# Optimization experiments

Measured on AMD Instinct MI355X. Metric: run time of the kernel, lower is better.

## Reference

```python
import jax, jax.numpy as jnp
import numpy as np

IN_F, OUT_F, N_TOK = 4096, 4096, 8192

def setup_inputs() -> dict:
    key = jax.random.key(0)
    k1, k2, k3 = jax.random.split(key, 3)
    x = jax.random.normal(k1, (N_TOK, IN_F), dtype=jnp.float32)
    scaler = jax.random.uniform(k2, (1,), dtype=jnp.float32)
    int8_weights = jax.random.randint(k3, (IN_F, OUT_F), -128, 128, dtype=jnp.int32)
    return {"x": x, "scaler": scaler, "int8_weights": int8_weights}

def reference(x, scaler, int8_weights):
    # dequantize int8 weights: fp_w = int8_w * scaler, then GEMM
    fp_weights = int8_weights.astype(x.dtype) * scaler  # [in, out]
    return jnp.matmul(x, fp_weights)  # [tokens, out]
```

## Files before the change

kernel.cpp:

```cpp
#include <hip/hip_runtime.h>

#define M_DIM 8192
#define N_DIM 4096
#define K_DIM 4096

typedef __attribute__((ext_vector_type(8))) __bf16 bf16x8;
typedef __attribute__((ext_vector_type(4))) float f32x4;
typedef __attribute__((ext_vector_type(8))) unsigned short u16x8;

typedef const __attribute__((address_space(1))) unsigned int gu32_t;
typedef __attribute__((address_space(3))) unsigned int lu32_t;

static __device__ __forceinline__ unsigned short f2bf(float f) {
    union { float f; unsigned int u; } v; v.f = f;
    unsigned int u = v.u;
    return (unsigned short)((u + 0x7fffu + ((u >> 16) & 1u)) >> 16);
}

#define X_BLOCKS 32768

__global__ __launch_bounds__(256) void prep_kernel(const float* __restrict__ x,
                                                   unsigned short* __restrict__ xb,
                                                   const int* __restrict__ w,
                                                   unsigned short* __restrict__ wt) {
    __shared__ unsigned short t[64][72];
    const int tid = threadIdx.x;
    if (blockIdx.x < X_BLOCKS) {
        size_t g = (size_t)blockIdx.x * 256 + tid;
        float4 a = ((const float4*)x)[g];
        ushort4 o;
        o.x = f2bf(a.x); o.y = f2bf(a.y); o.z = f2bf(a.z); o.w = f2bf(a.w);
        ((ushort4*)xb)[g] = o;
    } else {
        int bid = blockIdx.x - X_BLOCKS;
        int n0 = (bid & 63) * 64;
        int k0 = (bid >> 6) * 64;
#pragma unroll
        for (int i = 0; i < 16; i++) {
            int idx = tid + i * 256;
            int r = idx >> 6, c = idx & 63;
            int v = w[(size_t)(k0 + r) * N_DIM + n0 + c];
            t[c][r] = f2bf((float)v);
        }
        __syncthreads();
#pragma unroll
        for (int i = 0; i < 2; i++) {
            int slot = tid + i * 256;
            int r = slot >> 3, c = (slot & 7) * 8;
            u16x8 o = *(const u16x8*)&t[r][c];
            *(u16x8*)&wt[(size_t)(n0 + r) * K_DIM + k0 + c] = o;
        }
    }
}

static __device__ __forceinline__ int swz(int m) { return (m + (m >> 2)) & 3; }

__global__ __launch_bounds__(256) void gemm_bt_kernel(const unsigned short* __restrict__ A,
                                                      const unsigned short* __restrict__ B,
                                                      const float* __restrict__ scaler,
                                                      float* __restrict__ C) {
    __shared__ unsigned short As[128 * 32];
    __shared__ unsigned short Bs[128 * 32];

    const int tid  = threadIdx.x;
    const int m0   = blockIdx.y * 128;
    const int n0   = blockIdx.x * 128;
    const int wave = tid >> 6, lane = tid & 63;
    const int quad = lane >> 4, lr = lane & 15;
    const int wm   = wave >> 1, wn = wave & 1;

    const int q0 = tid, q1 = tid + 256;
    const int r0 = q0 >> 2, kc0 = (q0 & 3) ^ swz(r0);
    const int r1 = q1 >> 2, kc1 = (q1 & 3) ^ swz(r1);
    const unsigned short* ga0 = A + (size_t)(m0 + r0) * K_DIM + kc0 * 8;
    const unsigned short* ga1 = A + (size_t)(m0 + r1) * K_DIM + kc1 * 8;
    const unsigned short* gb0 = B + (size_t)(n0 + r0) * K_DIM + kc0 * 8;
    const unsigned short* gb1 = B + (size_t)(n0 + r1) * K_DIM + kc1 * 8;
    unsigned short* la0 = As + q0 * 8;
    unsigned short* la1 = As + q1 * 8;
    unsigned short* lb0 = Bs + q0 * 8;
    unsigned short* lb1 = Bs + q1 * 8;

    f32x4 acc[4][4];
#pragma unroll
    for (int i = 0; i < 4; i++)
#pragma unroll
        for (int j = 0; j < 4; j++) acc[i][j] = (f32x4){0.f, 0.f, 0.f, 0.f};

    const int swa = quad ^ swz(wm * 64 + lr);
    const int swb = quad ^ swz(wn * 64 + lr);
    const unsigned short* pa = &As[((wm * 64 + lr) * 4 + swa) * 8];
    const unsigned short* pb = &Bs[((wn * 64 + lr) * 4 + swb) * 8];

    for (int kt = 0; kt < K_DIM / 32; ++kt) {
        __builtin_amdgcn_global_load_lds((gu32_t*)ga0, (lu32_t*)la0, 16, 0, 0);
        __builtin_amdgcn_global_load_lds((gu32_t*)ga1, (lu32_t*)la1, 16, 0, 0);
        __builtin_amdgcn_global_load_lds((gu32_t*)gb0, (lu32_t*)lb0, 16, 0, 0);
        __builtin_amdgcn_global_load_lds((gu32_t*)gb1, (lu32_t*)lb1, 16, 0, 0);
        ga0 += 32; ga1 += 32; gb0 += 32; gb1 += 32;
        __syncthreads();

        bf16x8 af[4], bf[4];
#pragma unroll
        for (int mi = 0; mi < 4; mi++) af[mi] = *(const bf16x8*)(pa + mi * 512);
#pragma unroll
        for (int ni = 0; ni < 4; ni++) bf[ni] = *(const bf16x8*)(pb + ni * 512);

#pragma unroll
        for (int mi = 0; mi < 4; mi++)
#pragma unroll
            for (int ni = 0; ni < 4; ni++)
                acc[mi][ni] = __builtin_amdgcn_mfma_f32_16x16x32_bf16(
                    af[mi], bf[ni], acc[mi][ni], 0, 0, 0);
        __syncthreads();
    }

    const float s = scaler[0];
#pragma unroll
    for (int mi = 0; mi < 4; mi++)
#pragma unroll
        for (int ni = 0; ni < 4; ni++) {
            const int row = m0 + wm * 64 + mi * 16 + quad * 4;
            const int col = n0 + wn * 64 + ni * 16 + lr;
            float* cp = C + (size_t)row * N_DIM + col;
#pragma unroll
            for (int r = 0; r < 4; r++)
                cp[(size_t)r * N_DIM] = acc[mi][ni][r] * s;
        }
}

extern "C" void kernel_launch(void* const* d_in, const int* in_sizes, int n_in,
                              void* d_out, int out_size, void* d_ws, size_t ws_size,
                              hipStream_t stream) {
    const float* x      = (const float*)d_in[0];
    const float* scaler = (const float*)d_in[1];
    const int*   w      = (const int*)d_in[2];
    float*       out    = (float*)d_out;

    unsigned short* xb = (unsigned short*)d_ws;
    unsigned short* wt = xb + (size_t)M_DIM * K_DIM;

    prep_kernel<<<X_BLOCKS + (N_DIM / 64) * (K_DIM / 64), 256, 0, stream>>>(x, xb, w, wt);
    gemm_bt_kernel<<<dim3(N_DIM / 128, M_DIM / 128), 256, 0, stream>>>(xb, wt, scaler, out);
}
```

Baseline: 557.6 us.

## Replace GEMM with 256x256-tile double-buffered kernel and vectorize prep conversions

The 128x128 single-buffered GEMM is replaced by a 256x256-tile kernel with 512 threads, 8 waves, and a 128 KB LDS double-buffered pipeline. It uses XOR-swizzled LDS layout, manual waitcnt/barrier scheduling, s_setprio around MFMA bursts, and a grouped block-index remap for L2 locality. The prep kernel now converts 8 floats per thread and loads weights as int4 vectors, with the transpose done on the LDS read side. The aim is more data reuse per tile and overlap of global loads with MFMA work. In exchange the kernel needs high register and LDS use and depends on tightly hand-tuned synchronisation.

New measurement: 508.0 us. 1.1x faster.

```diff
diff --git a/kernel.cpp b/kernel.cpp
--- a/kernel.cpp
+++ b/kernel.cpp
@@ -7,6 +7,7 @@
 typedef __attribute__((ext_vector_type(8))) __bf16 bf16x8;
 typedef __attribute__((ext_vector_type(4))) float f32x4;
 typedef __attribute__((ext_vector_type(8))) unsigned short u16x8;
+typedef __attribute__((ext_vector_type(4))) unsigned short u16x4;
 
 typedef const __attribute__((address_space(1))) unsigned int gu32_t;
 typedef __attribute__((address_space(3))) unsigned int lu32_t;
@@ -17,116 +18,170 @@
     return (unsigned short)((u + 0x7fffu + ((u >> 16) & 1u)) >> 16);
 }
 
-#define X_BLOCKS 32768
+#define XBLOCKS 16384
 
 __global__ __launch_bounds__(256) void prep_kernel(const float* __restrict__ x,
                                                    unsigned short* __restrict__ xb,
                                                    const int* __restrict__ w,
                                                    unsigned short* __restrict__ wt) {
-    __shared__ unsigned short t[64][72];
+    __shared__ unsigned short t[64][68];
     const int tid = threadIdx.x;
-    if (blockIdx.x < X_BLOCKS) {
+    if (blockIdx.x < XBLOCKS) {
         size_t g = (size_t)blockIdx.x * 256 + tid;
-        float4 a = ((const float4*)x)[g];
-        ushort4 o;
-        o.x = f2bf(a.x); o.y = f2bf(a.y); o.z = f2bf(a.z); o.w = f2bf(a.w);
-        ((ushort4*)xb)[g] = o;
+        const float4* xp = (const float4*)x;
+        float4 a = xp[2 * g], b = xp[2 * g + 1];
+        u16x8 o;
+        o[0] = f2bf(a.x); o[1] = f2bf(a.y); o[2] = f2bf(a.z); o[3] = f2bf(a.w);
+        o[4] = f2bf(b.x); o[5] = f2bf(b.y); o[6] = f2bf(b.z); o[7] = f2bf(b.w);
+        *(u16x8*)&xb[g * 8] = o;
     } else {
-        int bid = blockIdx.x - X_BLOCKS;
-        int n0 = (bid & 63) * 64;
-        int k0 = (bid >> 6) * 64;
-#pragma unroll
-        for (int i = 0; i < 16; i++) {
-            int idx = tid + i * 256;
-            int r = idx >> 6, c = idx & 63;
-            int v = w[(size_t)(k0 + r) * N_DIM + n0 + c];
-            t[c][r] = f2bf((float)v);
+        const int bid = blockIdx.x - XBLOCKS;
+        const int n0 = (bid & 63) * 64;
+        const int k0 = (bid >> 6) * 64;
+#pragma unroll
+        for (int p = 0; p < 4; ++p) {
+            int r = p * 16 + (tid >> 4);
+            int c = (tid & 15) * 4;
+            int4 v = *(const int4*)&w[(size_t)(k0 + r) * N_DIM + n0 + c];
+            u16x4 o4;
+            o4[0] = f2bf((float)v.x); o4[1] = f2bf((float)v.y);
+            o4[2] = f2bf((float)v.z); o4[3] = f2bf((float)v.w);
+            *(u16x4*)&t[r][c] = o4;
         }
         __syncthreads();
 #pragma unroll
-        for (int i = 0; i < 2; i++) {
-            int slot = tid + i * 256;
-            int r = slot >> 3, c = (slot & 7) * 8;
-            u16x8 o = *(const u16x8*)&t[r][c];
-            *(u16x8*)&wt[(size_t)(n0 + r) * K_DIM + k0 + c] = o;
+        for (int p = 0; p < 2; ++p) {
+            int idx = p * 256 + tid;
+            int c  = idx >> 3;
+            int r0 = (idx & 7) * 8;
+            u16x8 o;
+#pragma unroll
+            for (int j = 0; j < 8; ++j) o[j] = t[r0 + j][c];
+            *(u16x8*)&wt[(size_t)(n0 + c) * K_DIM + k0 + r0] = o;
         }
     }
 }
 
-static __device__ __forceinline__ int swz(int m) { return (m + (m >> 2)) & 3; }
-
-__global__ __launch_bounds__(256) void gemm_bt_kernel(const unsigned short* __restrict__ A,
-                                                      const unsigned short* __restrict__ B,
-                                                      const float* __restrict__ scaler,
-                                                      float* __restrict__ C) {
-    __shared__ unsigned short As[128 * 32];
-    __shared__ unsigned short Bs[128 * 32];
-
-    const int tid  = threadIdx.x;
-    const int m0   = blockIdx.y * 128;
-    const int n0   = blockIdx.x * 128;
-    const int wave = tid >> 6, lane = tid & 63;
-    const int quad = lane >> 4, lr = lane & 15;
-    const int wm   = wave >> 1, wn = wave & 1;
-
-    const int q0 = tid, q1 = tid + 256;
-    const int r0 = q0 >> 2, kc0 = (q0 & 3) ^ swz(r0);
-    const int r1 = q1 >> 2, kc1 = (q1 & 3) ^ swz(r1);
-    const unsigned short* ga0 = A + (size_t)(m0 + r0) * K_DIM + kc0 * 8;
-    const unsigned short* ga1 = A + (size_t)(m0 + r1) * K_DIM + kc1 * 8;
-    const unsigned short* gb0 = B + (size_t)(n0 + r0) * K_DIM + kc0 * 8;
-    const unsigned short* gb1 = B + (size_t)(n0 + r1) * K_DIM + kc1 * 8;
-    unsigned short* la0 = As + q0 * 8;
-    unsigned short* la1 = As + q1 * 8;
-    unsigned short* lb0 = Bs + q0 * 8;
-    unsigned short* lb1 = Bs + q1 * 8;
-
-    f32x4 acc[4][4];
-#pragma unroll
-    for (int i = 0; i < 4; i++)
-#pragma unroll
-        for (int j = 0; j < 4; j++) acc[i][j] = (f32x4){0.f, 0.f, 0.f, 0.f};
-
-    const int swa = quad ^ swz(wm * 64 + lr);
-    const int swb = quad ^ swz(wn * 64 + lr);
-    const unsigned short* pa = &As[((wm * 64 + lr) * 4 + swa) * 8];
-    const unsigned short* pb = &Bs[((wn * 64 + lr) * 4 + swb) * 8];
-
-    for (int kt = 0; kt < K_DIM / 32; ++kt) {
-        __builtin_amdgcn_global_load_lds((gu32_t*)ga0, (lu32_t*)la0, 16, 0, 0);
-        __builtin_amdgcn_global_load_lds((gu32_t*)ga1, (lu32_t*)la1, 16, 0, 0);
-        __builtin_amdgcn_global_load_lds((gu32_t*)gb0, (lu32_t*)lb0, 16, 0, 0);
-        __builtin_amdgcn_global_load_lds((gu32_t*)gb1, (lu32_t*)lb1, 16, 0, 0);
-        ga0 += 32; ga1 += 32; gb0 += 32; gb1 += 32;
-        __syncthreads();
-
-        bf16x8 af[4], bf[4];
-#pragma unroll
-        for (int mi = 0; mi < 4; mi++) af[mi] = *(const bf16x8*)(pa + mi * 512);
-#pragma unroll
-        for (int ni = 0; ni < 4; ni++) bf[ni] = *(const bf16x8*)(pb + ni * 512);
-
-#pragma unroll
-        for (int mi = 0; mi < 4; mi++)
-#pragma unroll
-            for (int ni = 0; ni < 4; ni++)
-                acc[mi][ni] = __builtin_amdgcn_mfma_f32_16x16x32_bf16(
-                    af[mi], bf[ni], acc[mi][ni], 0, 0, 0);
-        __syncthreads();
+__global__ __launch_bounds__(512, 2) void gemm256_kernel(const unsigned short* __restrict__ A,
+                                                         const unsigned short* __restrict__ B,
+                                                         const float* __restrict__ scaler,
+                                                         float* __restrict__ C) {
+    __shared__ unsigned short sm[65536];
+
+    const int tid = threadIdx.x;
+
+    const int bid  = blockIdx.x;
+    const int sbid = (bid & 7) * 64 + (bid >> 3);
+    const int m0   = (sbid & 31) * 256;
+    const int n0   = (sbid >> 5) * 256;
+
+    const int lane = tid & 63, wave = tid >> 6;
+    const int lr   = lane & 15, quad = lane >> 4;
+    const int wm   = wave >> 2, wn = wave & 3;
+
+    const int d0 = tid * 16, d1 = d0 + 8192;
+    const int l0 = d0 ^ ((((d0 >> 7) & 1) << 4) | (((d0 >> 8) & 1) << 5) | (((d0 >> 9) & 1) << 6));
+    const int l1 = d1 ^ ((((d1 >> 7) & 1) << 4) | (((d1 >> 8) & 1) << 5) | (((d1 >> 9) & 1) << 6));
+    const int srow0 = l0 >> 6, scol0 = (l0 & 63) >> 1;
+    const int srow1 = l1 >> 6, scol1 = (l1 & 63) >> 1;
+    const unsigned short* gA0 = A + (size_t)(m0 + srow0) * K_DIM + scol0;
+    const unsigned short* gA1 = A + (size_t)(m0 + srow1) * K_DIM + scol1;
+    const unsigned short* gB0 = B + (size_t)(n0 + srow0) * K_DIM + scol0;
+    const unsigned short* gB1 = B + (size_t)(n0 + srow1) * K_DIM + scol1;
+    char* smc = (char*)sm;
+
+    const int amask = ((lr >> 1) & 7) << 4;
+    const int afo = (((wm * 128 + lr) * 64) + quad * 16) ^ amask;
+    const int bfo = (((wn * 64  + lr) * 64) + quad * 16) ^ amask;
+
+    f32x4 acc[8][4];
+#pragma unroll
+    for (int i = 0; i < 8; ++i)
+#pragma unroll
+        for (int j = 0; j < 4; ++j) acc[i][j] = (f32x4){0.f, 0.f, 0.f, 0.f};
+
+    bf16x8 af[4], bfr[4];
+
+#define STAGE_A(buf, kh, kt) do { const int _ko = (kt) * 64 + (kh) * 32; \
+    __builtin_amdgcn_global_load_lds((gu32_t*)(gA0 + _ko), (lu32_t*)(smc + ((buf)*4 + (kh)) * 16384 + d0), 16, 0, 0); \
+    __builtin_amdgcn_global_load_lds((gu32_t*)(gA1 + _ko), (lu32_t*)(smc + ((buf)*4 + (kh)) * 16384 + d1), 16, 0, 0); \
+} while (0)
+#define STAGE_B(buf, kh, kt) do { const int _ko = (kt) * 64 + (kh) * 32; \
+    __builtin_amdgcn_global_load_lds((gu32_t*)(gB0 + _ko), (lu32_t*)(smc + ((buf)*4 + 2 + (kh)) * 16384 + d0), 16, 0, 0); \
+    __builtin_amdgcn_global_load_lds((gu32_t*)(gB1 + _ko), (lu32_t*)(smc + ((buf)*4 + 2 + (kh)) * 16384 + d1), 16, 0, 0); \
+} while (0)
+#define LOADA(buf, kh, ch) do { const char* _p = smc + ((buf)*4 + (kh)) * 16384 + (ch) * 4096 + afo; \
+    _Pragma("unroll") for (int _mi = 0; _mi < 4; ++_mi) af[_mi] = *(const bf16x8*)(_p + _mi * 1024); \
+} while (0)
+#define LOADB(buf, kh) do { const char* _p = smc + ((buf)*4 + 2 + (kh)) * 16384 + bfo; \
+    _Pragma("unroll") for (int _ni = 0; _ni < 4; ++_ni) bfr[_ni] = *(const bf16x8*)(_p + _ni * 1024); \
+} while (0)
+#define MFMA16(ch) do { __builtin_amdgcn_s_setprio(1); \
+    _Pragma("unroll") for (int _mi = 0; _mi < 4; ++_mi) \
+    _Pragma("unroll") for (int _ni = 0; _ni < 4; ++_ni) \
+        acc[(ch)*4 + _mi][_ni] = __builtin_amdgcn_mfma_f32_16x16x32_bf16(af[_mi], bfr[_ni], acc[(ch)*4 + _mi][_ni], 0, 0, 0); \
+    __builtin_amdgcn_s_setprio(0); \
+} while (0)
+#define BARRIER __builtin_amdgcn_s_barrier()
+#define WAITL   asm volatile("s_waitcnt lgkmcnt(0)" ::: "memory")
+#define WAITV4  asm volatile("s_waitcnt vmcnt(4)" ::: "memory")
+
+    STAGE_A(0, 0, 0); STAGE_B(0, 0, 0);
+    STAGE_A(0, 1, 0); STAGE_B(0, 1, 0);
+    STAGE_A(1, 0, 1); STAGE_B(1, 0, 1);
+    asm volatile("s_waitcnt vmcnt(0)" ::: "memory");
+    BARRIER;
+
+    for (int i = 0; i < K_DIM / 128; ++i) {
+        const int t1 = 2 * i + 1;
+        LOADA(0, 0, 0); LOADB(0, 0);
+        STAGE_A(1, 1, t1);
+        BARRIER; WAITL; MFMA16(0); BARRIER;
+        LOADA(0, 0, 1);
+        STAGE_B(1, 1, t1);
+        BARRIER; WAITL; MFMA16(1); BARRIER;
+        LOADA(0, 1, 1); LOADB(0, 1);
+        STAGE_A(0, 0, (t1 + 1) & 63);
+        BARRIER; WAITL; MFMA16(1); BARRIER;
+        LOADA(0, 1, 0);
+        STAGE_B(0, 0, (t1 + 1) & 63);
+        BARRIER; WAITL; MFMA16(0); WAITV4; BARRIER;
+        LOADA(1, 0, 0); LOADB(1, 0);
+        STAGE_A(0, 1, (t1 + 1) & 63);
+        BARRIER; WAITL; MFMA16(0); BARRIER;
+        LOADA(1, 0, 1);
+        STAGE_B(0, 1, (t1 + 1) & 63);
+        BARRIER; WAITL; MFMA16(1); BARRIER;
+        LOADA(1, 1, 1); LOADB(1, 1);
+        STAGE_A(1, 0, (t1 + 2) & 63);
+        BARRIER; WAITL; MFMA16(1); BARRIER;
+        LOADA(1, 1, 0);
+        STAGE_B(1, 0, (t1 + 2) & 63);
+        BARRIER; WAITL; MFMA16(0); WAITV4; BARRIER;
     }
+    asm volatile("s_waitcnt vmcnt(0)" ::: "memory");
 
     const float s = scaler[0];
 #pragma unroll
-    for (int mi = 0; mi < 4; mi++)
-#pragma unroll
-        for (int ni = 0; ni < 4; ni++) {
-            const int row = m0 + wm * 64 + mi * 16 + quad * 4;
+    for (int mi = 0; mi < 8; ++mi)
+#pragma unroll
+        for (int ni = 0; ni < 4; ++ni) {
+            const int row = m0 + wm * 128 + mi * 16 + quad * 4;
             const int col = n0 + wn * 64 + ni * 16 + lr;
             float* cp = C + (size_t)row * N_DIM + col;
 #pragma unroll
-            for (int r = 0; r < 4; r++)
+            for (int r = 0; r < 4; ++r)
                 cp[(size_t)r * N_DIM] = acc[mi][ni][r] * s;
         }
+
+#undef STAGE_A
+#undef STAGE_B
+#undef LOADA
+#undef LOADB
+#undef MFMA16
+#undef BARRIER
+#undef WAITL
+#undef WAITV4
 }
 
 extern "C" void kernel_launch(void* const* d_in, const int* in_sizes, int n_in,
@@ -140,6 +195,6 @@
     unsigned short* xb = (unsigned short*)d_ws;
     unsigned short* wt = xb + (size_t)M_DIM * K_DIM;
 
-    prep_kernel<<<X_BLOCKS + (N_DIM / 64) * (K_DIM / 64), 256, 0, stream>>>(x, xb, w, wt);
-    gemm_bt_kernel<<<dim3(N_DIM / 128, M_DIM / 128), 256, 0, stream>>>(xb, wt, scaler, out);
-}
+    prep_kernel<<<XBLOCKS + (N_DIM / 64) * (K_DIM / 64), 256, 0, stream>>>(x, xb, w, wt);
+    gemm256_kernel<<<dim3((M_DIM / 256) * (N_DIM / 256)), 512, 0, stream>>>(xb, wt, scaler, out);
+}
```
